# Performance work log

Hardware: AMD Instinct MI355X
Metric: run time of the kernel (lower is better)

## Reference

```python
import jax, jax.numpy as jnp
import numpy as np

ISQRT2 = 0.7071067811865476  # 1/sqrt(2), haar analysis/synthesis coefficient
LEVELS = 13                  # pywt.dwt_max_level(8192, 'haar') = log2(8192)
J = 4                        # recursion_limit
BN_EPS = 1e-5


def haar_wavedec(x, levels):
    """Full-depth haar DWT (mode='zero' is exact for power-of-2 length).
    x: [..., N]. Returns bank [cA_L, cD_L, cD_{L-1}, ..., cD_1] (pywt order).
    Vectorized over batch AND channel dims at once (the per-channel python
    loop in the torch module computes identical math per channel)."""
    a = x
    details = []
    for _ in range(levels):
        even, odd = a[..., ::2], a[..., 1::2]
        details.append((even - odd) * ISQRT2)
        a = (even + odd) * ISQRT2
    return [a] + details[::-1]


def haar_waverec(bank):
    """Inverse of haar_wavedec; bank in pywt order [cA, cD_coarse..cD_fine]."""
    a = bank[0]
    for d in bank[1:]:
        up = jnp.stack([a + d, a - d], axis=-1) * ISQRT2  # interleave even/odd
        a = up.reshape(a.shape[:-1] + (a.shape[-1] * 2,))
    return a


def batch_norm_train(y, g, b):
    # BatchNorm1d training mode: stats over (batch, length) per channel, biased var
    mean = jnp.mean(y, axis=(0, 2), keepdims=True)
    var = jnp.var(y, axis=(0, 2), keepdims=True)
    return (y - mean) * jax.lax.rsqrt(var + BN_EPS) * g[None, :, None] + b[None, :, None]


def reference(x, gamma, beta):
    # x: [B, C, N]; gamma, beta: [J, C]
    bank = haar_wavedec(x, LEVELS)  # computed once, reused for all masks
    zeros_bank = [jnp.zeros_like(c) for c in bank]

    # masked_inputs[j]: IWT keeping only band j (pool_inputs=False -> full bank)
    masked_inputs = []
    for j in range(J):
        mb = [bank[i] if i == j else zeros_bank[i] for i in range(len(bank))]
        masked_inputs.append(haar_waverec(mb))

    # masked_targets[j]: IWT keeping bands 0..j (pool_targets=False)
    masked_targets = []
    for j in range(J):
        mb = [bank[i] if i <= j else zeros_bank[i] for i in range(len(bank))]
        masked_targets.append(haar_waverec(mb))

    # per-level BatchNorm on inputs only
    masked_inputs = [batch_norm_train(masked_inputs[j], gamma[j], beta[j]) for j in range(J)]

    # stack for a single output tensor: [2, J, B, C, N]
    return jnp.stack([jnp.stack(masked_inputs), jnp.stack(masked_targets)])


def setup_inputs() -> dict:
    key = jax.random.key(0)
    x = jax.random.normal(key, (64, 16, 8192), dtype=jnp.float32)
    gamma = jnp.ones((J, 16), dtype=jnp.float32)
    beta = jnp.zeros((J, 16), dtype=jnp.float32)
    return {"x": x, "gamma": gamma, "beta": beta}
```

## Files before the change

### kernel.cpp

```cpp
#include <hip/hip_runtime.h>


#define NROWS 1024
#define ROWLEN 8192
#define STATS_STRIDE 16

__global__ __launch_bounds__(256) void row_stats_kernel(const float* __restrict__ x,
                                                        float* __restrict__ stats) {
    int row = blockIdx.x;
    const float4* xr = reinterpret_cast<const float4*>(x) + (size_t)row * (ROWLEN / 4);
    int t = threadIdx.x;
    float s[8];
#pragma unroll
    for (int k = 0; k < 8; ++k) {
        float4 v = xr[t + 256 * k];
        s[k] = (v.x + v.y) + (v.z + v.w);
    }
    __shared__ float red[8][4];
    __shared__ float m3s[8];
    int lane = t & 63, wave = t >> 6;
#pragma unroll
    for (int k = 0; k < 8; ++k) {
        float v = s[k];
#pragma unroll
        for (int off = 32; off; off >>= 1) v += __shfl_down(v, off, 64);
        if (lane == 0) red[k][wave] = v;
    }
    __syncthreads();
    if (t < 8) m3s[t] = (red[t][0] + red[t][1] + red[t][2] + red[t][3]) * (1.0f / 1024.0f);
    __syncthreads();
    if (t == 0) {
        float* o = stats + (size_t)row * STATS_STRIDE;
        float m2[4], m1[2];
#pragma unroll
        for (int k = 0; k < 4; ++k) m2[k] = 0.5f * (m3s[2 * k] + m3s[2 * k + 1]);
        m1[0] = 0.5f * (m2[0] + m2[1]);
        m1[1] = 0.5f * (m2[2] + m2[3]);
        float m0 = 0.5f * (m1[0] + m1[1]);
        o[0] = m0;
        o[1] = m1[0]; o[2] = m1[1];
        o[3] = m2[0]; o[4] = m2[1]; o[5] = m2[2]; o[6] = m2[3];
#pragma unroll
        for (int k = 0; k < 8; ++k) o[7 + k] = m3s[k];
    }
}

__global__ __launch_bounds__(64) void bn_stats_kernel(const float* __restrict__ stats,
                                                      const float* __restrict__ gamma,
                                                      const float* __restrict__ beta,
                                                      float* __restrict__ bn ) {
    int j = blockIdx.x >> 4;
    int c = blockIdx.x & 15;
    int b = threadIdx.x;
    const float* s = stats + (size_t)((b << 4) + c) * STATS_STRIDE;
    float sum = 0.f, sum2 = 0.f;
    float B = (float)(ROWLEN >> j);
    if (j == 0) {
        float d = s[0];
        sum = d; sum2 = d * d;
    } else {
        int base = (1 << j) - 1;
        int pbase = (1 << (j - 1)) - 1;
        int nb = 1 << j;
        for (int k = 0; k < nb; ++k) {
            float d = s[base + k] - s[pbase + (k >> 1)];
            sum += d; sum2 += d * d;
        }
    }
    sum *= B; sum2 *= B;
#pragma unroll
    for (int off = 32; off; off >>= 1) {
        sum  += __shfl_down(sum, off, 64);
        sum2 += __shfl_down(sum2, off, 64);
    }
    if (b == 0) {
        const float N = 64.0f * 8192.0f;
        float mean = sum / N;
        float var = sum2 / N - mean * mean;
        float inv = rsqrtf(var + 1e-5f);
        float scale = gamma[(j << 4) + c] * inv;
        float shift = beta[(j << 4) + c] - mean * scale;
        bn[((j << 4) + c) * 2 + 0] = scale;
        bn[((j << 4) + c) * 2 + 1] = shift;
    }
}

__global__ __launch_bounds__(256) void write_out_kernel(const float* __restrict__ stats,
                                                        const float* __restrict__ bn,
                                                        float4* __restrict__ out) {
    unsigned idx = blockIdx.x * blockDim.x + threadIdx.x;
    unsigned stride = gridDim.x * blockDim.x;
    const unsigned total = 1u << 24;
    for (unsigned i = idx; i < total; i += stride) {
        unsigned e = i << 2;
        unsigned n = e & 8191u;
        unsigned c = (e >> 13) & 15u;
        unsigned b = (e >> 17) & 63u;
        unsigned j = (e >> 23) & 3u;
        unsigned part = (e >> 25) & 1u;
        const float* s = stats + (size_t)((b << 4) + c) * STATS_STRIDE;
        float mj = s[(1u << j) - 1u + (n >> (13u - j))];
        float val;
        if (part) {
            val = mj;
        } else {
            float d = mj;
            if (j > 0) d -= s[(1u << (j - 1u)) - 1u + (n >> (14u - j))];
            unsigned jc = (j << 4) + c;
            val = d * bn[jc * 2] + bn[jc * 2 + 1];
        }
        out[i] = make_float4(val, val, val, val);
    }
}

extern "C" void kernel_launch(void* const* d_in, const int* in_sizes, int n_in,
                              void* d_out, int out_size, void* d_ws, size_t ws_size,
                              hipStream_t stream) {
    const float* x     = (const float*)d_in[0];
    const float* gamma = (const float*)d_in[1];
    const float* beta  = (const float*)d_in[2];
    float* out = (float*)d_out;

    float* stats = (float*)d_ws;
    float* bn    = stats + (size_t)NROWS * STATS_STRIDE;

    row_stats_kernel<<<NROWS, 256, 0, stream>>>(x, stats);
    bn_stats_kernel<<<64, 64, 0, stream>>>(stats, gamma, beta, bn);
    write_out_kernel<<<2048, 256, 0, stream>>>(stats, bn, (float4*)out);
}
```

Before: 62.11 us.

## Restructure output writer to one block per row with nontemporal loads and stores

```diff
diff --git a/kernel.cpp b/kernel.cpp
--- a/kernel.cpp
+++ b/kernel.cpp
@@ -5,15 +5,17 @@
 #define ROWLEN 8192
 #define STATS_STRIDE 16
 
+typedef float f32x4 __attribute__((ext_vector_type(4)));
+
 __global__ __launch_bounds__(256) void row_stats_kernel(const float* __restrict__ x,
                                                         float* __restrict__ stats) {
     int row = blockIdx.x;
-    const float4* xr = reinterpret_cast<const float4*>(x) + (size_t)row * (ROWLEN / 4);
+    const f32x4* xr = reinterpret_cast<const f32x4*>(x) + (size_t)row * (ROWLEN / 4);
     int t = threadIdx.x;
     float s[8];
 #pragma unroll
     for (int k = 0; k < 8; ++k) {
-        float4 v = xr[t + 256 * k];
+        f32x4 v = __builtin_nontemporal_load(&xr[t + 256 * k]);
         s[k] = (v.x + v.y) + (v.z + v.w);
     }
     __shared__ float red[8][4];
@@ -87,29 +89,37 @@
 
 __global__ __launch_bounds__(256) void write_out_kernel(const float* __restrict__ stats,
                                                         const float* __restrict__ bn,
-                                                        float4* __restrict__ out) {
-    unsigned idx = blockIdx.x * blockDim.x + threadIdx.x;
-    unsigned stride = gridDim.x * blockDim.x;
-    const unsigned total = 1u << 24;
-    for (unsigned i = idx; i < total; i += stride) {
-        unsigned e = i << 2;
-        unsigned n = e & 8191u;
-        unsigned c = (e >> 13) & 15u;
-        unsigned b = (e >> 17) & 63u;
-        unsigned j = (e >> 23) & 3u;
-        unsigned part = (e >> 25) & 1u;
+                                                        f32x4* __restrict__ out) {
+    unsigned blk = blockIdx.x;
+    unsigned c = blk & 15u;
+    unsigned b = (blk >> 4) & 63u;
+    unsigned j = (blk >> 10) & 3u;
+    unsigned part = blk >> 12;
+    unsigned nb = 1u << j;
+    unsigned t = threadIdx.x;
+    __shared__ float sv[8];
+    if (t < nb) {
         const float* s = stats + (size_t)((b << 4) + c) * STATS_STRIDE;
-        float mj = s[(1u << j) - 1u + (n >> (13u - j))];
-        float val;
+        float mj = s[nb - 1u + t];
+        float v;
         if (part) {
-            val = mj;
+            v = mj;
         } else {
             float d = mj;
-            if (j > 0) d -= s[(1u << (j - 1u)) - 1u + (n >> (14u - j))];
+            if (j > 0) d -= s[(nb >> 1) - 1u + (t >> 1)];
             unsigned jc = (j << 4) + c;
-            val = d * bn[jc * 2] + bn[jc * 2 + 1];
+            v = d * bn[jc * 2] + bn[jc * 2 + 1];
         }
-        out[i] = make_float4(val, val, val, val);
+        sv[t] = v;
+    }
+    __syncthreads();
+    f32x4* orow = out + (size_t)blk * 2048;
+    unsigned sh = 3u - j;
+#pragma unroll
+    for (unsigned i = 0; i < 8; ++i) {
+        float v = sv[i >> sh];
+        f32x4 q = {v, v, v, v};
+        __builtin_nontemporal_store(q, &orow[t + (i << 8)]);
     }
 }
 
@@ -126,5 +136,5 @@
 
     row_stats_kernel<<<NROWS, 256, 0, stream>>>(x, stats);
     bn_stats_kernel<<<64, 64, 0, stream>>>(stats, gamma, beta, bn);
-    write_out_kernel<<<2048, 256, 0, stream>>>(stats, bn, (float4*)out);
+    write_out_kernel<<<8192, 256, 0, stream>>>(stats, bn, (f32x4*)out);
 }
```

Result: no change. 62.23 us (+0.2%).
